# Kernel tuning notes

Hardware: AMD Instinct MI355X
Metric: run time of the kernel (lower is better)

## Reference

```python
import jax, jax.numpy as jnp
import numpy as np

KERNEL_MUL = 2.0
KERNEL_NUM = 5
FIX_SIGMA = None


def setup_inputs() -> dict:
    key = jax.random.key(0)
    k1, k2 = jax.random.split(key)
    source = jax.random.normal(k1, (4096, 512), dtype=jnp.float32)
    target = jax.random.normal(k2, (4096, 512), dtype=jnp.float32)
    return {"source": source, "target": target}


def reference(source, target):
    batch_size = source.shape[0]
    total = jnp.concatenate([source, target], axis=0)  # [N, D], N = n1 + n2
    n_samples = total.shape[0]

    # Pairwise squared L2 distances via Gram-matrix trick (same math as
    # the explicit NxNxD broadcast in the original, without materializing it).
    sq = jnp.sum(total * total, axis=1)               # [N]
    gram = total @ total.T                            # [N, N]
    l2 = sq[:, None] + sq[None, :] - 2.0 * gram       # [N, N]

    if FIX_SIGMA:
        bandwidth = jnp.asarray(FIX_SIGMA, dtype=l2.dtype)
    else:
        # torch used L2_distance.data -> no gradient through bandwidth
        bandwidth = jax.lax.stop_gradient(jnp.sum(l2)) / (n_samples ** 2 - n_samples)
    bandwidth = bandwidth / (KERNEL_MUL ** (KERNEL_NUM // 2))

    # Multi-bandwidth Gaussian kernel sum
    kernels = jnp.zeros_like(l2)
    for i in range(KERNEL_NUM):
        kernels = kernels + jnp.exp(-l2 / (bandwidth * (KERNEL_MUL ** i)))

    b = batch_size
    XX = kernels[:b, :b]
    YY = kernels[b:, b:]
    XY = kernels[:b, b:]
    YX = kernels[b:, :b]
    loss = jnp.mean(XX + YY - XY - YX)
    return loss
```

## Files before the change

### kernel.cpp

```cpp
#include <hip/hip_runtime.h>
#include <math.h>

typedef float f32x4 __attribute__((ext_vector_type(4)));
typedef int   i32x4 __attribute__((ext_vector_type(4)));
typedef signed char i8x8 __attribute__((ext_vector_type(8)));

#define NROWS 8192
#define NCOLS 512
#define BHALF 4096
#define NT    64
#define NBLK  2080
#define CSPART 256
#define QS    24.0f
#define INV_S2 (1.0f / (24.0f * 24.0f))

__global__ void k_conv(const float* __restrict__ src, const float* __restrict__ tgt,
                       signed char* __restrict__ bfrag, float* __restrict__ sq,
                       int* __restrict__ sqi, float* __restrict__ cspart) {
    __shared__ signed char ldsc[32][528];
    __shared__ float colp[4][NCOLS];
    int t = threadIdx.x, w = t >> 6, l = t & 63;
    int r0 = blockIdx.x * 32;
    float c0x=0.f,c0y=0.f,c0z=0.f,c0w=0.f, c1x=0.f,c1y=0.f,c1z=0.f,c1w=0.f;
    #pragma unroll
    for (int r = 0; r < 8; ++r) {
        int row = r0 + w * 8 + r;
        const float* base = (row < BHALF) ? (src + (size_t)row * NCOLS)
                                          : (tgt + (size_t)(row - BHALF) * NCOLS);
        float4 a = ((const float4*)base)[2 * l];
        float4 b = ((const float4*)base)[2 * l + 1];
        int q0 = (int)rintf(fminf(fmaxf(a.x * QS, -127.f), 127.f));
        int q1 = (int)rintf(fminf(fmaxf(a.y * QS, -127.f), 127.f));
        int q2 = (int)rintf(fminf(fmaxf(a.z * QS, -127.f), 127.f));
        int q3 = (int)rintf(fminf(fmaxf(a.w * QS, -127.f), 127.f));
        int q4 = (int)rintf(fminf(fmaxf(b.x * QS, -127.f), 127.f));
        int q5 = (int)rintf(fminf(fmaxf(b.y * QS, -127.f), 127.f));
        int q6 = (int)rintf(fminf(fmaxf(b.z * QS, -127.f), 127.f));
        int q7 = (int)rintf(fminf(fmaxf(b.w * QS, -127.f), 127.f));
        i8x8 v8;
        v8[0]=(signed char)q0; v8[1]=(signed char)q1; v8[2]=(signed char)q2; v8[3]=(signed char)q3;
        v8[4]=(signed char)q4; v8[5]=(signed char)q5; v8[6]=(signed char)q6; v8[7]=(signed char)q7;
        *(i8x8*)&ldsc[w * 8 + r][l * 8] = v8;
        float s = a.x*a.x + a.y*a.y + a.z*a.z + a.w*a.w
                + b.x*b.x + b.y*b.y + b.z*b.z + b.w*b.w;
        int si = q0*q0 + q1*q1 + q2*q2 + q3*q3 + q4*q4 + q5*q5 + q6*q6 + q7*q7;
        #pragma unroll
        for (int o = 32; o > 0; o >>= 1) {
            s  += __shfl_down(s, o);
            si += __shfl_down(si, o);
        }
        if (l == 0) { sq[row] = s; sqi[row] = si; }
        c0x += a.x; c0y += a.y; c0z += a.z; c0w += a.w;
        c1x += b.x; c1y += b.y; c1z += b.z; c1w += b.w;
    }
    colp[w][l*8+0] = c0x; colp[w][l*8+1] = c0y; colp[w][l*8+2] = c0z; colp[w][l*8+3] = c0w;
    colp[w][l*8+4] = c1x; colp[w][l*8+5] = c1y; colp[w][l*8+6] = c1z; colp[w][l*8+7] = c1w;
    __syncthreads();
    float s0 = colp[0][t] + colp[1][t] + colp[2][t] + colp[3][t];
    float s1 = colp[0][t+256] + colp[1][t+256] + colp[2][t+256] + colp[3][t+256];
    cspart[(size_t)blockIdx.x * NCOLS + t]       = s0;
    cspart[(size_t)blockIdx.x * NCOLS + t + 256] = s1;
    int rg0 = blockIdx.x * 2;
    #pragma unroll
    for (int c4 = 0; c4 < 4; ++c4) {
        int c = c4 * 256 + t;
        int g = c >> 9, sl = (c >> 4) & 31, lrr = c & 15;
        i32x4 v = *(const i32x4*)&ldsc[g * 16 + lrr][sl * 16];
        *(i32x4*)(bfrag + (size_t)(rg0 + g) * 8192 + sl * 256 + lrr * 16) = v;
    }
}

__global__ void k_bw(const float* __restrict__ sq, const float* __restrict__ cspart,
                     float* __restrict__ cvals) {
    __shared__ double red[1024];
    int t = threadIdx.x;
    double a = 0.0;
    #pragma unroll
    for (int i = 0; i < 8; ++i) a += (double)sq[t + i * 1024];
    red[t] = a; __syncthreads();
    for (int o = 512; o > 0; o >>= 1) { if (t < o) red[t] += red[t + o]; __syncthreads(); }
    double sT = red[0];
    __syncthreads();
    int c = t & 511, h = t >> 9;
    double d0 = 0.0, d1 = 0.0, d2 = 0.0, d3 = 0.0;
    int p0 = h * 128;
    #pragma unroll 8
    for (int p = 0; p < 128; p += 4) {
        d0 += (double)cspart[(size_t)(p0 + p + 0) * NCOLS + c];
        d1 += (double)cspart[(size_t)(p0 + p + 1) * NCOLS + c];
        d2 += (double)cspart[(size_t)(p0 + p + 2) * NCOLS + c];
        d3 += (double)cspart[(size_t)(p0 + p + 3) * NCOLS + c];
    }
    red[t] = (d0 + d1) + (d2 + d3);
    __syncthreads();
    double v = 0.0;
    if (t < 512) { double cs = red[t] + red[t + 512]; v = cs * cs; }
    __syncthreads();
    red[t] = v; __syncthreads();
    for (int o = 512; o > 0; o >>= 1) { if (t < o) red[t] += red[t + o]; __syncthreads(); }
    if (t == 0) {
        double G = red[0];
        double sum_l2 = 2.0 * (double)NROWS * sT - 2.0 * G;
        double denom = (double)NROWS * (double)NROWS - (double)NROWS;
        double bw = sum_l2 / denom / 4.0;
        const double L2E = 1.4426950408889634;
        double b = bw;
        #pragma unroll
        for (int k = 0; k < 5; ++k) { cvals[k] = (float)(L2E / b); b *= 2.0; }
    }
}

__global__ __launch_bounds__(256, 3)
void k_mmd(const signed char* __restrict__ bfrag, const int* __restrict__ sqi,
           const float* __restrict__ cvals, double* __restrict__ psum) {
    __shared__ float wred[4];

    int bid = blockIdx.x;
    int swz = (bid & 7) * (NBLK / 8) + (bid >> 3);
    int rem = swz;
    int I = 0;
    while (rem >= NT - I) { rem -= NT - I; ++I; }
    int J = I + rem;

    const int t  = threadIdx.x;
    const int w  = t >> 6;
    const int l  = t & 63;
    const int lr = l & 15;
    const int lk = l >> 4;

    const bool dsup = (I == J);
    int da, db;
    if (dsup) { da = (w == 2) ? 1 : 0; db = (w == 0) ? 0 : 1; }
    else      { da = w >> 1;           db = w & 1; }
    const int i_t = 2 * I + da, j_t = 2 * J + db;
    const int rowA0 = i_t * 64, rowB0 = j_t * 64;

    const int i_u = __builtin_amdgcn_readfirstlane(i_t);
    const int j_u = __builtin_amdgcn_readfirstlane(j_t);
    const signed char* bA = bfrag + (size_t)i_u * 32768;
    const signed char* bB = bfrag + (size_t)j_u * 32768;
    const int voff = lk * 256 + lr * 16;

    i32x4 acc[4][4] = {};
    i32x4 afP[4], bfP[4], afQ[4], bfQ[4];

    #define LOADF(afX, bfX, kt)                                                    \
        _Pragma("unroll")                                                          \
        for (int m = 0; m < 4; ++m)                                                \
            afX[m] = *(const i32x4*)(bA + m * 8192 + (kt) * 1024 + voff);          \
        _Pragma("unroll")                                                          \
        for (int n = 0; n < 4; ++n)                                                \
            bfX[n] = *(const i32x4*)(bB + n * 8192 + (kt) * 1024 + voff);

    #define MM(afX, bfX)                                                           \
        _Pragma("unroll")                                                          \
        for (int m = 0; m < 4; ++m)                                                \
            _Pragma("unroll")                                                      \
            for (int n = 0; n < 4; ++n)                                            \
                acc[m][n] = __builtin_amdgcn_mfma_i32_16x16x64_i8(                 \
                    afX[m], bfX[n], acc[m][n], 0, 0, 0);

    LOADF(afP, bfP, 0)
    LOADF(afQ, bfQ, 1)
    MM(afP, bfP)
    LOADF(afP, bfP, 2)
    MM(afQ, bfQ)
    LOADF(afQ, bfQ, 3)
    MM(afP, bfP)
    LOADF(afP, bfP, 4)
    MM(afQ, bfQ)
    LOADF(afQ, bfQ, 5)
    MM(afP, bfP)
    LOADF(afP, bfP, 6)
    MM(afQ, bfQ)
    LOADF(afQ, bfQ, 7)
    MM(afP, bfP)
    MM(afQ, bfQ)

    #undef LOADF
    #undef MM

    i32x4 sqa[4];
    #pragma unroll
    for (int m = 0; m < 4; ++m)
        sqa[m] = *(const i32x4*)&sqi[rowA0 + m * 16 + lk * 4];
    int sqb[4];
    #pragma unroll
    for (int n = 0; n < 4; ++n)
        sqb[n] = sqi[rowB0 + n * 16 + lr];
    float c4i = cvals[4] * INV_S2;

    const bool elem = dsup && ((w & 1) == 0);
    const float wb  = dsup ? 1.f : 2.f;
    const float sgn = ((rowA0 < BHALF) == (rowB0 < BHALF)) ? 1.f : -1.f;
    float local = 0.f;
    #pragma unroll
    for (int m = 0; m < 4; ++m)
        #pragma unroll
        for (int n = 0; n < 4; ++n)
            #pragma unroll
            for (int r = 0; r < 4; ++r) {
                int   d   = acc[m][n][r];
                int   l2i = sqa[m][r] + sqb[n] - 2 * d;
                float l2  = (float)l2i;
                float x  = exp2f(-l2 * c4i);
                float x2 = x * x;
                float x4 = x2 * x2;
                float x8 = x4 * x4;
                float e  = x + x2 + x4 + x8 + x8 * x8;
                if (elem) {
                    int gi = rowA0 + m * 16 + lk * 4 + r;
                    int gj = rowB0 + n * 16 + lr;
                    float wgt = (gj > gi) ? 2.f : ((gj == gi) ? 1.f : 0.f);
                    local += wgt * e;
                } else {
                    local += e;
                }
            }
    if (!elem) local *= wb * sgn;

    #pragma unroll
    for (int o = 32; o > 0; o >>= 1) local += __shfl_down(local, o);
    if (l == 0) wred[w] = local;
    __syncthreads();
    if (t == 0) {
        psum[blockIdx.x] = (double)((wred[0] + wred[1]) + (wred[2] + wred[3]));
    }
}

__global__ void k_final(const double* __restrict__ psum, float* __restrict__ out) {
    __shared__ double red[256];
    int t = threadIdx.x;
    double a = 0.0;
    for (int i = t; i < NBLK; i += 256) a += psum[i];
    red[t] = a; __syncthreads();
    for (int o = 128; o > 0; o >>= 1) { if (t < o) red[t] += red[t + o]; __syncthreads(); }
    if (t == 0) out[0] = (float)(red[0] * (1.0 / ((double)BHALF * (double)BHALF)));
}

extern "C" void kernel_launch(void* const* d_in, const int* in_sizes, int n_in,
                              void* d_out, int out_size, void* d_ws, size_t ws_size,
                              hipStream_t stream) {
    (void)in_sizes; (void)n_in; (void)out_size; (void)ws_size;
    const float* src = (const float*)d_in[0];
    const float* tgt = (const float*)d_in[1];
    float* out = (float*)d_out;
    char* ws = (char*)d_ws;
    signed char* bfrag = (signed char*)(ws);
    float*  sq     = (float*) (ws + 4194304);
    int*    sqi    = (int*)   (ws + 4194304 + 32768);
    float*  cspart = (float*) (ws + 4194304 + 65536);
    float*  cvals  = (float*) (ws + 4194304 + 65536 + 524288);
    double* psum   = (double*)(ws + 4194304 + 65536 + 524288 + 32);

    k_conv  <<<CSPART, 256, 0, stream>>>(src, tgt, bfrag, sq, sqi, cspart);
    k_bw    <<<1, 1024, 0, stream>>>(sq, cspart, cvals);
    k_mmd   <<<NBLK, 256, 0, stream>>>(bfrag, sqi, cvals, psum);
    k_final <<<1, 256, 0, stream>>>(psum, out);
}
```

Before: 66.59 us.

## Split MMD work into single-wave blocks over 64x64 triangular tiles

The 128x128 super-tile blocks of four waves become one-wave blocks, each computing one 64x64 tile of the upper triangle, so 8256 blocks launch instead of 2080. The diagonal-tile special casing across waves, the shared-memory reduction and the barrier are removed. Each block now writes its partial sum directly. exp2f is also replaced with the hardware exp2 builtin. In exchange there are more blocks and more psum entries for the final reduction, and operand reuse across waves sharing the same rows is lost.

```diff
diff --git a/kernel.cpp b/kernel.cpp
--- a/kernel.cpp
+++ b/kernel.cpp
@@ -8,8 +8,8 @@
 #define NROWS 8192
 #define NCOLS 512
 #define BHALF 4096
-#define NT    64
-#define NBLK  2080
+#define NTT   128
+#define NBLK  8256
 #define CSPART 256
 #define QS    24.0f
 #define INV_S2 (1.0f / (24.0f * 24.0f))
@@ -110,33 +110,24 @@
     }
 }
 
-__global__ __launch_bounds__(256, 3)
+__global__ __launch_bounds__(64, 3)
 void k_mmd(const signed char* __restrict__ bfrag, const int* __restrict__ sqi,
            const float* __restrict__ cvals, double* __restrict__ psum) {
-    __shared__ float wred[4];
-
     int bid = blockIdx.x;
     int swz = (bid & 7) * (NBLK / 8) + (bid >> 3);
     int rem = swz;
     int I = 0;
-    while (rem >= NT - I) { rem -= NT - I; ++I; }
+    while (rem >= NTT - I) { rem -= NTT - I; ++I; }
     int J = I + rem;
 
-    const int t  = threadIdx.x;
-    const int w  = t >> 6;
-    const int l  = t & 63;
+    const int l  = threadIdx.x;
     const int lr = l & 15;
     const int lk = l >> 4;
 
-    const bool dsup = (I == J);
-    int da, db;
-    if (dsup) { da = (w == 2) ? 1 : 0; db = (w == 0) ? 0 : 1; }
-    else      { da = w >> 1;           db = w & 1; }
-    const int i_t = 2 * I + da, j_t = 2 * J + db;
-    const int rowA0 = i_t * 64, rowB0 = j_t * 64;
-
-    const int i_u = __builtin_amdgcn_readfirstlane(i_t);
-    const int j_u = __builtin_amdgcn_readfirstlane(j_t);
+    const int rowA0 = I * 64, rowB0 = J * 64;
+
+    const int i_u = __builtin_amdgcn_readfirstlane(I);
+    const int j_u = __builtin_amdgcn_readfirstlane(J);
     const signed char* bA = bfrag + (size_t)i_u * 32768;
     const signed char* bB = bfrag + (size_t)j_u * 32768;
     const int voff = lk * 256 + lr * 16;
@@ -190,8 +181,7 @@
         sqb[n] = sqi[rowB0 + n * 16 + lr];
     float c4i = cvals[4] * INV_S2;
 
-    const bool elem = dsup && ((w & 1) == 0);
-    const float wb  = dsup ? 1.f : 2.f;
+    const bool diag = (I == J);
     const float sgn = ((rowA0 < BHALF) == (rowB0 < BHALF)) ? 1.f : -1.f;
     float local = 0.f;
     #pragma unroll
@@ -203,12 +193,12 @@
                 int   d   = acc[m][n][r];
                 int   l2i = sqa[m][r] + sqb[n] - 2 * d;
                 float l2  = (float)l2i;
-                float x  = exp2f(-l2 * c4i);
+                float x  = __builtin_amdgcn_exp2f(-l2 * c4i);
                 float x2 = x * x;
                 float x4 = x2 * x2;
                 float x8 = x4 * x4;
                 float e  = x + x2 + x4 + x8 + x8 * x8;
-                if (elem) {
+                if (diag) {
                     int gi = rowA0 + m * 16 + lk * 4 + r;
                     int gj = rowB0 + n * 16 + lr;
                     float wgt = (gj > gi) ? 2.f : ((gj == gi) ? 1.f : 0.f);
@@ -217,15 +207,11 @@
                     local += e;
                 }
             }
-    if (!elem) local *= wb * sgn;
+    if (!diag) local *= 2.f * sgn;
 
     #pragma unroll
     for (int o = 32; o > 0; o >>= 1) local += __shfl_down(local, o);
-    if (l == 0) wred[w] = local;
-    __syncthreads();
-    if (t == 0) {
-        psum[blockIdx.x] = (double)((wred[0] + wred[1]) + (wred[2] + wred[3]));
-    }
+    if (l == 0) psum[blockIdx.x] = (double)local;
 }
 
 __global__ void k_final(const double* __restrict__ psum, float* __restrict__ out) {
@@ -255,6 +241,6 @@
 
     k_conv  <<<CSPART, 256, 0, stream>>>(src, tgt, bfrag, sq, sqi, cspart);
     k_bw    <<<1, 1024, 0, stream>>>(sq, cspart, cvals);
-    k_mmd   <<<NBLK, 256, 0, stream>>>(bfrag, sqi, cvals, psum);
+    k_mmd   <<<NBLK, 64, 0, stream>>>(bfrag, sqi, cvals, psum);
     k_final <<<1, 256, 0, stream>>>(psum, out);
 }
```

Result: slower. 70.25 us (+5.5%).
